# Kernel optimization log

Measured on AMD Instinct MI355X. Metric: run time of the kernel, lower is better.

Reference implementation:

```python
import jax, jax.numpy as jnp
import numpy as np

S, B, D, H, DH = 2048, 2, 512, 8, 64
SCALE = 1.0 / DH ** 0.5
EPS = 1e-5
LN_EPS = 1e-5


def setup_inputs() -> dict:
    key = jax.random.key(0)
    k1, k2, k3, k4 = jax.random.split(key, 4)
    h = jax.random.normal(k1, (S, B, D), dtype=jnp.float32)
    # causal mask, True = masked out, shape [qlen, klen, 1] (dim==3 branch)
    attn_mask = jnp.triu(jnp.ones((S, S), dtype=bool), k=1)[:, :, None]
    Wq = jax.random.normal(k2, (D, H * DH), dtype=jnp.float32) * 0.02
    Wkv = jax.random.normal(k3, (D, 2 * H * DH), dtype=jnp.float32) * 0.02
    Wo = jax.random.normal(k4, (H * DH, D), dtype=jnp.float32) * 0.02
    gamma = jnp.ones((D,), dtype=jnp.float32)
    beta = jnp.zeros((D,), dtype=jnp.float32)
    return {"h": h, "Wq": Wq, "Wkv": Wkv, "Wo": Wo,
            "gamma": gamma, "beta": beta, "attn_mask": attn_mask}


def _layer_norm(x, gamma, beta):
    mu = jnp.mean(x, axis=-1, keepdims=True)
    var = jnp.mean(jnp.square(x - mu), axis=-1, keepdims=True)
    return (x - mu) * jax.lax.rsqrt(var + LN_EPS) * gamma + beta


def reference(h, Wq, Wkv, Wo, gamma, beta, attn_mask):
    # mems=None, pre_lnorm=False, dropout=dropatt=0 (eval)
    c = h
    head_q = (h @ Wq).reshape(S, B, H, DH)
    kv = (c @ Wkv)
    head_k, head_v = jnp.split(kv, 2, axis=-1)
    head_k = head_k.reshape(S, B, H, DH)
    head_v = head_v.reshape(S, B, H, DH)
    # elu(x) + 1 feature map
    head_q = jax.nn.elu(head_q) + 1.0
    head_k = jax.nn.elu(head_k) + 1.0
    # quadratic score matrix [i, j, b, n]
    attn_score = jnp.einsum('ibnd,jbnd->ijbn', head_q, head_k) * SCALE
    # dim==3 mask: [qlen, klen, 1] -> [qlen, klen, 1, 1], fill with 0
    attn_score = jnp.where(attn_mask[:, :, :, None], 0.0, attn_score)
    # sum-normalize over key axis (dim 1 = j)
    denominator = jnp.sum(attn_score, axis=1, keepdims=True) + EPS
    attn_prob = attn_score / denominator
    attn_vec = jnp.einsum('ijbn,jbnd->ibnd', attn_prob, head_v)
    attn_vec = attn_vec.reshape(S, B, H * DH)
    attn_out = attn_vec @ Wo
    # post-lnorm residual
    return _layer_norm(h + attn_out, gamma, beta)
```

## Files before the change

kernel.cpp:

```cpp
#include <hip/hip_runtime.h>
#include <hip/hip_bf16.h>
#include <math.h>

#define SCALE 0.125f
#define EPS 1e-5f
#define LN_EPS 1e-5f

typedef short short8 __attribute__((ext_vector_type(8)));
typedef float floatx4 __attribute__((ext_vector_type(4)));
typedef unsigned short us;

__device__ __forceinline__ float elu1(float x) { return x > 0.f ? x + 1.f : __expf(x); }
__device__ __forceinline__ us f2bf(float f) {
    __hip_bfloat16 b = __float2bfloat16(f);
    return __builtin_bit_cast(us, b);
}
__device__ __forceinline__ void gload_lds16(const void* g, void* lds) {
    __builtin_amdgcn_global_load_lds(
        (const __attribute__((address_space(1))) unsigned int*)g,
        (__attribute__((address_space(3))) unsigned int*)lds, 16, 0, 0);
}
__device__ __forceinline__ floatx4 mfma_bf16(short8 a, short8 b, floatx4 c) {
    return __builtin_amdgcn_mfma_f32_16x16x32_bf16(a, b, c, 0, 0, 0);
}

__global__ __launch_bounds__(256)
void pack_kernel(const float* __restrict__ h, const float* __restrict__ Wq,
                 const float* __restrict__ Wkv, const float* __restrict__ Wo,
                 us* __restrict__ hB, us* __restrict__ WqkvT, us* __restrict__ WoT,
                 us* __restrict__ VTg) {
    const int idx = (blockIdx.x * 256 + threadIdx.x) * 4;
    if (idx < 2097152) {
        float4 v = *(const float4*)(h + idx);
        ushort4 o;
        o.x = f2bf(v.x); o.y = f2bf(v.y); o.z = f2bf(v.z); o.w = f2bf(v.w);
        *(ushort4*)(hB + idx) = o;
    } else if (idx < 2883584) {
        int e = idx - 2097152;
        int n = e >> 9, k = e & 511;
        const float* src; int ld, col;
        if (n < 512) { src = Wq; ld = 512; col = n; }
        else         { src = Wkv; ld = 1024; col = n - 512; }
        ushort4 o;
        o.x = f2bf(src[(size_t)(k + 0) * ld + col]);
        o.y = f2bf(src[(size_t)(k + 1) * ld + col]);
        o.z = f2bf(src[(size_t)(k + 2) * ld + col]);
        o.w = f2bf(src[(size_t)(k + 3) * ld + col]);
        *(ushort4*)(WqkvT + e) = o;
    } else if (idx < 3145728) {
        int e = idx - 2883584;
        int n = e >> 9, k = e & 511;
        ushort4 o;
        o.x = f2bf(Wo[(size_t)(k + 0) * 512 + n]);
        o.y = f2bf(Wo[(size_t)(k + 1) * 512 + n]);
        o.z = f2bf(Wo[(size_t)(k + 2) * 512 + n]);
        o.w = f2bf(Wo[(size_t)(k + 3) * 512 + n]);
        *(ushort4*)(WoT + e) = o;
    } else if (idx < 3178496) {
        int e = idx - 3145728;
        int chain = e >> 11, s = e & 2047;
        ushort4 o; o.x = 0x3f80; o.y = 0x3f80; o.z = 0x3f80; o.w = 0x3f80;
        *(ushort4*)(VTg + ((size_t)(chain * 80 + 64)) * 2048 + s) = o;
    }
}

__global__ __launch_bounds__(256)
void qkv_gemm(const us* __restrict__ A, const us* __restrict__ BT,
              us* __restrict__ Qg, us* __restrict__ Kg, us* __restrict__ Vg) {
    __shared__ __align__(16) us As[128 * 32];
    __shared__ __align__(16) us Bs[128 * 32];
    const int tid = threadIdx.x;
    const int w = tid >> 6, l = tid & 63;
    const int m0 = blockIdx.y * 128, n0 = blockIdx.x * 128;
    const int wm = (w >> 1) * 64, wn = (w & 1) * 64;
    floatx4 acc[4][4];
#pragma unroll
    for (int i = 0; i < 4; ++i)
#pragma unroll
        for (int j = 0; j < 4; ++j)
#pragma unroll
            for (int e = 0; e < 4; ++e) acc[i][j][e] = 0.f;

    for (int kt = 0; kt < 512; kt += 32) {
        __syncthreads();
#pragma unroll
        for (int r = 0; r < 2; ++r) {
            int slot = (r * 4 + w) * 64 + l;
            int row = slot >> 2, part = slot & 3;
            int g = part ^ (row & 3);
            gload_lds16(A + (size_t)(m0 + row) * 512 + kt + g * 8, As + (r * 4 + w) * 512);
            gload_lds16(BT + (size_t)(n0 + row) * 512 + kt + g * 8, Bs + (r * 4 + w) * 512);
        }
        __syncthreads();
        short8 a[4], b[4];
#pragma unroll
        for (int mi = 0; mi < 4; ++mi) {
            int row = wm + mi * 16 + (l & 15);
            int p = (l >> 4) ^ (row & 3);
            a[mi] = *(const short8*)(As + row * 32 + p * 8);
        }
#pragma unroll
        for (int ni = 0; ni < 4; ++ni) {
            int row = wn + ni * 16 + (l & 15);
            int p = (l >> 4) ^ (row & 3);
            b[ni] = *(const short8*)(Bs + row * 32 + p * 8);
        }
#pragma unroll
        for (int mi = 0; mi < 4; ++mi)
#pragma unroll
            for (int ni = 0; ni < 4; ++ni)
                acc[mi][ni] = mfma_bf16(a[mi], b[ni], acc[mi][ni]);
    }
    const int region = blockIdx.x >> 2;
    us* outp = region == 0 ? Qg : (region == 1 ? Kg : Vg);
    const int cb = n0 - region * 512;
#pragma unroll
    for (int mi = 0; mi < 4; ++mi)
#pragma unroll
        for (int ni = 0; ni < 4; ++ni)
#pragma unroll
            for (int r = 0; r < 4; ++r) {
                int row = m0 + wm + mi * 16 + (l >> 4) * 4 + r;
                int col = cb + wn + ni * 16 + (l & 15);
                float v = acc[mi][ni][r];
                if (region < 2) v = elu1(v);
                outp[(size_t)row * 512 + col] = f2bf(v);
            }
}

__global__ __launch_bounds__(256)
void chunk_kv_kernel(const us* __restrict__ Kg, const us* __restrict__ Vg,
                     float* __restrict__ KVc, us* __restrict__ VTg) {
    __shared__ __align__(16) us VT_l[80 * 72];
    __shared__ __align__(16) us KT_l[64 * 72];
    const int c = blockIdx.x, chain = blockIdx.y;
    const int b = chain >> 3, hh = chain & 7;
    const int tid = threadIdx.x;
    const int w = tid >> 6, l = tid & 63;
#pragma unroll
    for (int gi = 0; gi < 2; ++gi) {
        int g = w + gi * 4;
        __align__(16) us vv[8];
        __align__(16) us kk[8];
#pragma unroll
        for (int e = 0; e < 8; ++e) {
            size_t off = (size_t)((c * 64 + g * 8 + e) * 2 + b) * 512 + hh * 64 + l;
            vv[e] = Vg[off];
            kk[e] = Kg[off];
        }
        *(uint4*)(VT_l + l * 72 + g * 8) = *(uint4*)vv;
        *(uint4*)(KT_l + l * 72 + g * 8) = *(uint4*)kk;
        *(uint4*)(VTg + ((size_t)(chain * 80 + l)) * 2048 + c * 64 + g * 8) = *(uint4*)vv;
    }
    if (tid < 8) {
        ushort4 o; o.x = 0x3f80; o.y = 0x3f80; o.z = 0x3f80; o.w = 0x3f80;
        *(ushort4*)(VT_l + 64 * 72 + tid * 8) = o;
        *(ushort4*)(VT_l + 64 * 72 + tid * 8 + 4) = o;
    }
    __syncthreads();
    const int l15 = l & 15, l4 = l >> 4;
    short8 af[5][2], bfr[2];
#pragma unroll
    for (int mi = 0; mi < 5; ++mi) {
        int row = mi * 16 + l15;
        af[mi][0] = *(const short8*)(VT_l + row * 72 + l4 * 8);
        af[mi][1] = *(const short8*)(VT_l + row * 72 + 32 + l4 * 8);
    }
    {
        int row = w * 16 + l15;
        bfr[0] = *(const short8*)(KT_l + row * 72 + l4 * 8);
        bfr[1] = *(const short8*)(KT_l + row * 72 + 32 + l4 * 8);
    }
    float* out = KVc + (size_t)(chain * 32 + c) * 4608;
#pragma unroll
    for (int mi = 0; mi < 5; ++mi) {
        floatx4 a = {0.f, 0.f, 0.f, 0.f};
        a = mfma_bf16(af[mi][0], bfr[0], a);
        a = mfma_bf16(af[mi][1], bfr[1], a);
#pragma unroll
        for (int r = 0; r < 4; ++r) {
            int row = mi * 16 + l4 * 4 + r;
            if (row < 65) out[row * 64 + w * 16 + l15] = a[r];
        }
    }
}

__global__ __launch_bounds__(256)
void cumsum_kernel(const float* __restrict__ KVc, us* __restrict__ MTg) {
    const int chain = blockIdx.x, rg = blockIdx.y;
    const int row = rg * 4 + (threadIdx.x >> 6), col = threadIdx.x & 63;
    const float* in = KVc + (size_t)chain * 32 * 4608 + row * 64 + col;
    us* out = MTg + ((size_t)chain * 32 * 80 + row) * 64 + col;
    float acc = 0.f;
#pragma unroll 4
    for (int cc = 0; cc < 32; ++cc) {
        out[(size_t)cc * 5120] = f2bf(acc);
        acc += in[(size_t)cc * 4608];
    }
}

__global__ __launch_bounds__(256)
void attn_kernel(const us* __restrict__ Qg, const us* __restrict__ Kg,
                 const us* __restrict__ VTg, const us* __restrict__ MTg,
                 us* __restrict__ ATT) {
    __shared__ __align__(16) us Sl[64 * 64];
    const int c = blockIdx.x, chain = blockIdx.y;
    const int b = chain >> 3, hh = chain & 7;
    const int tid = threadIdx.x;
    const int w = tid >> 6, l = tid & 63;
    const int l15 = l & 15, l4 = l >> 4;

    short8 qf[2];
    {
        const us* qb = Qg + ((size_t)((c * 64 + w * 16 + l15) * 2 + b)) * 512 + hh * 64 + l4 * 8;
        qf[0] = *(const short8*)(qb);
        qf[1] = *(const short8*)(qb + 32);
    }
    short8 kf[4][2];
#pragma unroll
    for (int ni = 0; ni < 4; ++ni) {
        const us* kb = Kg + ((size_t)((c * 64 + ni * 16 + l15) * 2 + b)) * 512 + hh * 64 + l4 * 8;
        kf[ni][0] = *(const short8*)(kb);
        kf[ni][1] = *(const short8*)(kb + 32);
    }
    short8 vf[5][2];
#pragma unroll
    for (int ni = 0; ni < 5; ++ni) {
        const us* vb = VTg + ((size_t)(chain * 80 + ni * 16 + l15)) * 2048 + c * 64 + l4 * 8;
        vf[ni][0] = *(const short8*)(vb);
        vf[ni][1] = *(const short8*)(vb + 32);
    }
    short8 mf[5][2];
#pragma unroll
    for (int ni = 0; ni < 5; ++ni) {
        const us* mb = MTg + ((size_t)((chain * 32 + c) * 80 + ni * 16 + l15)) * 64 + l4 * 8;
        mf[ni][0] = *(const short8*)(mb);
        mf[ni][1] = *(const short8*)(mb + 32);
    }

    const int ibase = w * 16 + l4 * 4;
#pragma unroll
    for (int ni = 0; ni < 4; ++ni) {
        floatx4 s = {0.f, 0.f, 0.f, 0.f};
        s = mfma_bf16(qf[0], kf[ni][0], s);
        s = mfma_bf16(qf[1], kf[ni][1], s);
        int col = ni * 16 + l15;
#pragma unroll
        for (int r = 0; r < 4; ++r) {
            int i = ibase + r;
            float v = (col <= i) ? s[r] : 0.f;
            Sl[i * 64 + (((col >> 3) ^ (i & 7)) * 8) + (col & 7)] = f2bf(v);
        }
    }
    __syncthreads();

    short8 sf[2];
    {
        int ir = w * 16 + l15;
        sf[0] = *(const short8*)(Sl + ir * 64 + ((l4 ^ (ir & 7)) * 8));
        sf[1] = *(const short8*)(Sl + ir * 64 + (((4 + l4) ^ (ir & 7)) * 8));
    }

    floatx4 acc[5];
#pragma unroll
    for (int ni = 0; ni < 5; ++ni) {
        floatx4 a = {0.f, 0.f, 0.f, 0.f};
        a = mfma_bf16(sf[0], vf[ni][0], a);
        a = mfma_bf16(sf[1], vf[ni][1], a);
        a = mfma_bf16(qf[0], mf[ni][0], a);
        a = mfma_bf16(qf[1], mf[ni][1], a);
        acc[ni] = a;
    }

    float fac[4];
#pragma unroll
    for (int r = 0; r < 4; ++r) {
        float den = __shfl(acc[4][r], l & 48, 64);
        fac[r] = SCALE / (SCALE * den + EPS);
    }
#pragma unroll
    for (int ni = 0; ni < 4; ++ni)
#pragma unroll
        for (int r = 0; r < 4; ++r) {
            int i = ibase + r;
            ATT[((size_t)((c * 64 + i) * 2 + b)) * 512 + hh * 64 + ni * 16 + l15] =
                f2bf(acc[ni][r] * fac[r]);
        }
}

template <typename OUTT, int ELU_LIM>
__global__ __launch_bounds__(256)
void gemm_mfma(const us* __restrict__ A, const us* __restrict__ BT,
               OUTT* __restrict__ C, int M, int N, int K) {
    __shared__ __align__(16) us As[128 * 32];
    __shared__ __align__(16) us Bs[128 * 32];
    const int tid = threadIdx.x;
    const int w = tid >> 6, l = tid & 63;
    const int m0 = blockIdx.y * 128, n0 = blockIdx.x * 128;
    const int wm = (w >> 1) * 64, wn = (w & 1) * 64;
    floatx4 acc[4][4];
#pragma unroll
    for (int i = 0; i < 4; ++i)
#pragma unroll
        for (int j = 0; j < 4; ++j)
#pragma unroll
            for (int e = 0; e < 4; ++e) acc[i][j][e] = 0.f;
    for (int kt = 0; kt < K; kt += 32) {
        __syncthreads();
#pragma unroll
        for (int r = 0; r < 2; ++r) {
            int slot = (r * 4 + w) * 64 + l;
            int row = slot >> 2, part = slot & 3;
            int g = part ^ (row & 3);
            gload_lds16(A + (size_t)(m0 + row) * K + kt + g * 8, As + (r * 4 + w) * 512);
            gload_lds16(BT + (size_t)(n0 + row) * K + kt + g * 8, Bs + (r * 4 + w) * 512);
        }
        __syncthreads();
        short8 a[4], b[4];
#pragma unroll
        for (int mi = 0; mi < 4; ++mi) {
            int row = wm + mi * 16 + (l & 15);
            int p = (l >> 4) ^ (row & 3);
            a[mi] = *(const short8*)(As + row * 32 + p * 8);
        }
#pragma unroll
        for (int ni = 0; ni < 4; ++ni) {
            int row = wn + ni * 16 + (l & 15);
            int p = (l >> 4) ^ (row & 3);
            b[ni] = *(const short8*)(Bs + row * 32 + p * 8);
        }
#pragma unroll
        for (int mi = 0; mi < 4; ++mi)
#pragma unroll
            for (int ni = 0; ni < 4; ++ni)
                acc[mi][ni] = mfma_bf16(a[mi], b[ni], acc[mi][ni]);
    }
#pragma unroll
    for (int mi = 0; mi < 4; ++mi)
#pragma unroll
        for (int ni = 0; ni < 4; ++ni)
#pragma unroll
            for (int r = 0; r < 4; ++r) {
                int row = m0 + wm + mi * 16 + (l >> 4) * 4 + r;
                int col = n0 + wn + ni * 16 + (l & 15);
                float v = acc[mi][ni][r];
                if (col < ELU_LIM) v = elu1(v);
                if constexpr (sizeof(OUTT) == 2)
                    C[(size_t)row * N + col] = (OUTT)f2bf(v);
                else
                    C[(size_t)row * N + col] = (OUTT)v;
            }
}

__global__ __launch_bounds__(256)
void ln_kernel(const float* __restrict__ h, const float* __restrict__ AO,
               const float* __restrict__ gamma, const float* __restrict__ beta,
               float* __restrict__ out) {
    const int tid = threadIdx.x;
    const int lane = tid & 63, wave = tid >> 6;
    const int row = blockIdx.x * 4 + wave;
    float v[8];
    float sum = 0.f;
#pragma unroll
    for (int i = 0; i < 8; ++i) {
        int col = lane + i * 64;
        float x = h[(size_t)row * 512 + col] + AO[(size_t)row * 512 + col];
        v[i] = x;
        sum += x;
    }
#pragma unroll
    for (int off = 32; off >= 1; off >>= 1) sum += __shfl_xor(sum, off, 64);
    float mean = sum * (1.f / 512);
    float var = 0.f;
#pragma unroll
    for (int i = 0; i < 8; ++i) {
        float d = v[i] - mean;
        var = fmaf(d, d, var);
    }
#pragma unroll
    for (int off = 32; off >= 1; off >>= 1) var += __shfl_xor(var, off, 64);
    float rstd = rsqrtf(var * (1.f / 512) + LN_EPS);
#pragma unroll
    for (int i = 0; i < 8; ++i) {
        int col = lane + i * 64;
        out[(size_t)row * 512 + col] = (v[i] - mean) * rstd * gamma[col] + beta[col];
    }
}

extern "C" void kernel_launch(void* const* d_in, const int* in_sizes, int n_in,
                              void* d_out, int out_size, void* d_ws, size_t ws_size,
                              hipStream_t stream) {
    const float* h = (const float*)d_in[0];
    const float* Wq = (const float*)d_in[1];
    const float* Wkv = (const float*)d_in[2];
    const float* Wo = (const float*)d_in[3];
    const float* gamma = (const float*)d_in[4];
    const float* beta = (const float*)d_in[5];

    char* ws = (char*)d_ws;
    us* Qg      = (us*)(ws + 0);
    us* Kg      = (us*)(ws + 4194304);
    us* Vg      = (us*)(ws + 8388608);
    us* VTg     = (us*)(ws + 12582912);
    us* ATT     = (us*)(ws + 17825792);
    us* WoT     = (us*)(ws + 22020096);
    us* MTg     = (us*)(ws + 22544384);
    us* hB      = (us*)(ws + 27787264);
    us* WqkvT   = (us*)(ws + 31981568);
    float* KVc  = (float*)(ws + 27787264);
    float* AO   = (float*)(ws + 0);

    dim3 blk(256);
    pack_kernel<<<3104, blk, 0, stream>>>(h, Wq, Wkv, Wo, hB, WqkvT, WoT, VTg);
    qkv_gemm<<<dim3(12, 32), blk, 0, stream>>>(hB, WqkvT, Qg, Kg, Vg);
    chunk_kv_kernel<<<dim3(32, 16), blk, 0, stream>>>(Kg, Vg, KVc, VTg);
    cumsum_kernel<<<dim3(16, 17), blk, 0, stream>>>(KVc, MTg);
    attn_kernel<<<dim3(32, 16), blk, 0, stream>>>(Qg, Kg, VTg, MTg, ATT);
    gemm_mfma<float, 0><<<dim3(4, 32), blk, 0, stream>>>(ATT, WoT, AO, 4096, 512, 512);
    ln_kernel<<<1024, blk, 0, stream>>>(h, AO, gamma, beta, (float*)d_out);
}
```

Baseline: 147.1 us.

## Fuse Wo GEMM with LayerNorm, tile weight transpose, stage attention operands in LDS

```diff
diff --git a/kernel.cpp b/kernel.cpp
--- a/kernel.cpp
+++ b/kernel.cpp
@@ -29,35 +29,57 @@
                  const float* __restrict__ Wkv, const float* __restrict__ Wo,
                  us* __restrict__ hB, us* __restrict__ WqkvT, us* __restrict__ WoT,
                  us* __restrict__ VTg) {
-    const int idx = (blockIdx.x * 256 + threadIdx.x) * 4;
-    if (idx < 2097152) {
+    const int bid = blockIdx.x, tid = threadIdx.x;
+    if (bid < 2048) {
+        int idx = bid * 1024 + tid * 4;
         float4 v = *(const float4*)(h + idx);
         ushort4 o;
         o.x = f2bf(v.x); o.y = f2bf(v.y); o.z = f2bf(v.z); o.w = f2bf(v.w);
         *(ushort4*)(hB + idx) = o;
-    } else if (idx < 2883584) {
-        int e = idx - 2097152;
-        int n = e >> 9, k = e & 511;
-        const float* src; int ld, col;
-        if (n < 512) { src = Wq; ld = 512; col = n; }
-        else         { src = Wkv; ld = 1024; col = n - 512; }
-        ushort4 o;
-        o.x = f2bf(src[(size_t)(k + 0) * ld + col]);
-        o.y = f2bf(src[(size_t)(k + 1) * ld + col]);
-        o.z = f2bf(src[(size_t)(k + 2) * ld + col]);
-        o.w = f2bf(src[(size_t)(k + 3) * ld + col]);
-        *(ushort4*)(WqkvT + e) = o;
-    } else if (idx < 3145728) {
-        int e = idx - 2883584;
-        int n = e >> 9, k = e & 511;
-        ushort4 o;
-        o.x = f2bf(Wo[(size_t)(k + 0) * 512 + n]);
-        o.y = f2bf(Wo[(size_t)(k + 1) * 512 + n]);
-        o.z = f2bf(Wo[(size_t)(k + 2) * 512 + n]);
-        o.w = f2bf(Wo[(size_t)(k + 3) * 512 + n]);
-        *(ushort4*)(WoT + e) = o;
-    } else if (idx < 3178496) {
-        int e = idx - 3145728;
+        return;
+    }
+    if (bid < 2304) {
+        __shared__ us T[64][72];
+        const float* src; int ld, n0s, k0; us* dst;
+        if (bid < 2240) {
+            int t2 = bid - 2048;
+            int nt = t2 % 24, kt = t2 / 24;
+            int n0 = nt * 64; k0 = kt * 64;
+            if (n0 < 512) { src = Wq; ld = 512; n0s = n0; }
+            else          { src = Wkv; ld = 1024; n0s = n0 - 512; }
+            dst = WqkvT + (size_t)n0 * 512;
+        } else {
+            int t2 = bid - 2240;
+            int nt = t2 & 7, kt = t2 >> 3;
+            src = Wo; ld = 512; n0s = nt * 64; k0 = kt * 64;
+            dst = WoT + (size_t)(nt * 64) * 512;
+        }
+        {
+            int k = tid >> 2, cs = (tid & 3) * 16;
+            const float* p = src + (size_t)(k0 + k) * ld + n0s + cs;
+#pragma unroll
+            for (int q = 0; q < 4; ++q) {
+                float4 v = *(const float4*)(p + q * 4);
+                T[k][cs + q * 4 + 0] = f2bf(v.x);
+                T[k][cs + q * 4 + 1] = f2bf(v.y);
+                T[k][cs + q * 4 + 2] = f2bf(v.z);
+                T[k][cs + q * 4 + 3] = f2bf(v.w);
+            }
+        }
+        __syncthreads();
+        {
+            int n = tid >> 2, ks = (tid & 3) * 16;
+            __align__(16) us tmp[16];
+#pragma unroll
+            for (int j = 0; j < 16; ++j) tmp[j] = T[ks + j][n];
+            us* po = dst + (size_t)n * 512 + k0 + ks;
+            *(uint4*)(po) = *(uint4*)(tmp);
+            *(uint4*)(po + 8) = *(uint4*)(tmp + 8);
+        }
+        return;
+    }
+    {
+        int e = (bid - 2304) * 1024 + tid * 4;
         int chain = e >> 11, s = e & 2047;
         ushort4 o; o.x = 0x3f80; o.y = 0x3f80; o.z = 0x3f80; o.w = 0x3f80;
         *(ushort4*)(VTg + ((size_t)(chain * 80 + 64)) * 2048 + s) = o;
@@ -203,39 +225,62 @@
 void attn_kernel(const us* __restrict__ Qg, const us* __restrict__ Kg,
                  const us* __restrict__ VTg, const us* __restrict__ MTg,
                  us* __restrict__ ATT) {
+    __shared__ __align__(16) us Qs[64 * 64];
+    __shared__ __align__(16) us Ks[64 * 64];
+    __shared__ __align__(16) us Vs[80 * 64];
+    __shared__ __align__(16) us Ms[80 * 64];
     __shared__ __align__(16) us Sl[64 * 64];
     const int c = blockIdx.x, chain = blockIdx.y;
     const int b = chain >> 3, hh = chain & 7;
     const int tid = threadIdx.x;
     const int w = tid >> 6, l = tid & 63;
     const int l15 = l & 15, l4 = l >> 4;
+    const int lrow = l >> 3, lg = l & 7;
+
+#pragma unroll
+    for (int r = 0; r < 2; ++r) {
+        int slot = r * 4 + w;
+        int row = slot * 8 + lrow;
+        int g = lg ^ (row & 7);
+        size_t grow = (size_t)((c * 64 + row) * 2 + b) * 512 + hh * 64 + g * 8;
+        gload_lds16(Qg + grow, Qs + slot * 512);
+        gload_lds16(Kg + grow, Ks + slot * 512);
+    }
+#pragma unroll
+    for (int r = 0; r < 3; ++r) {
+        int slot = r * 4 + w;
+        if (slot < 10) {
+            int row = slot * 8 + lrow;
+            int g = lg ^ (row & 7);
+            gload_lds16(VTg + (size_t)(chain * 80 + row) * 2048 + c * 64 + g * 8,
+                        Vs + slot * 512);
+            gload_lds16(MTg + ((size_t)(chain * 32 + c) * 80 + row) * 64 + g * 8,
+                        Ms + slot * 512);
+        }
+    }
+    __syncthreads();
 
     short8 qf[2];
     {
-        const us* qb = Qg + ((size_t)((c * 64 + w * 16 + l15) * 2 + b)) * 512 + hh * 64 + l4 * 8;
-        qf[0] = *(const short8*)(qb);
-        qf[1] = *(const short8*)(qb + 32);
+        int row = w * 16 + l15, p = l4 ^ (row & 7);
+        qf[0] = *(const short8*)(Qs + row * 64 + p * 8);
+        qf[1] = *(const short8*)(Qs + row * 64 + (p ^ 4) * 8);
     }
     short8 kf[4][2];
 #pragma unroll
     for (int ni = 0; ni < 4; ++ni) {
-        const us* kb = Kg + ((size_t)((c * 64 + ni * 16 + l15) * 2 + b)) * 512 + hh * 64 + l4 * 8;
-        kf[ni][0] = *(const short8*)(kb);
-        kf[ni][1] = *(const short8*)(kb + 32);
-    }
-    short8 vf[5][2];
+        int row = ni * 16 + l15, p = l4 ^ (row & 7);
+        kf[ni][0] = *(const short8*)(Ks + row * 64 + p * 8);
+        kf[ni][1] = *(const short8*)(Ks + row * 64 + (p ^ 4) * 8);
+    }
+    short8 vf[5][2], mf[5][2];
 #pragma unroll
     for (int ni = 0; ni < 5; ++ni) {
-        const us* vb = VTg + ((size_t)(chain * 80 + ni * 16 + l15)) * 2048 + c * 64 + l4 * 8;
-        vf[ni][0] = *(const short8*)(vb);
-        vf[ni][1] = *(const short8*)(vb + 32);
-    }
-    short8 mf[5][2];
-#pragma unroll
-    for (int ni = 0; ni < 5; ++ni) {
-        const us* mb = MTg + ((size_t)((chain * 32 + c) * 80 + ni * 16 + l15)) * 64 + l4 * 8;
-        mf[ni][0] = *(const short8*)(mb);
-        mf[ni][1] = *(const short8*)(mb + 32);
+        int row = ni * 16 + l15, p = l4 ^ (row & 7);
+        vf[ni][0] = *(const short8*)(Vs + row * 64 + p * 8);
+        vf[ni][1] = *(const short8*)(Vs + row * 64 + (p ^ 4) * 8);
+        mf[ni][0] = *(const short8*)(Ms + row * 64 + p * 8);
+        mf[ni][1] = *(const short8*)(Ms + row * 64 + (p ^ 4) * 8);
     }
 
     const int ibase = w * 16 + l4 * 4;
@@ -288,103 +333,104 @@
         }
 }
 
-template <typename OUTT, int ELU_LIM>
-__global__ __launch_bounds__(256)
-void gemm_mfma(const us* __restrict__ A, const us* __restrict__ BT,
-               OUTT* __restrict__ C, int M, int N, int K) {
-    __shared__ __align__(16) us As[128 * 32];
-    __shared__ __align__(16) us Bs[128 * 32];
+__global__ __launch_bounds__(256)
+void wo_ln_kernel(const us* __restrict__ ATT, const us* __restrict__ WoT,
+                  const float* __restrict__ h, const float* __restrict__ gamma,
+                  const float* __restrict__ beta, float* __restrict__ out) {
+    __shared__ __align__(16) us As[32 * 32];
+    __shared__ __align__(16) us Bs[512 * 32];
+    __shared__ float redS[4][32];
+    __shared__ float redQ[4][32];
+    __shared__ float mml[32], rsl[32];
     const int tid = threadIdx.x;
     const int w = tid >> 6, l = tid & 63;
-    const int m0 = blockIdx.y * 128, n0 = blockIdx.x * 128;
-    const int wm = (w >> 1) * 64, wn = (w & 1) * 64;
-    floatx4 acc[4][4];
-#pragma unroll
-    for (int i = 0; i < 4; ++i)
-#pragma unroll
-        for (int j = 0; j < 4; ++j)
+    const int l15 = l & 15, l4 = l >> 4;
+    const int m0 = blockIdx.x * 32, wn = w * 128;
+    floatx4 acc[2][8];
+#pragma unroll
+    for (int i = 0; i < 2; ++i)
+#pragma unroll
+        for (int j = 0; j < 8; ++j)
 #pragma unroll
             for (int e = 0; e < 4; ++e) acc[i][j][e] = 0.f;
-    for (int kt = 0; kt < K; kt += 32) {
+
+    for (int kt = 0; kt < 512; kt += 32) {
         __syncthreads();
 #pragma unroll
-        for (int r = 0; r < 2; ++r) {
-            int slot = (r * 4 + w) * 64 + l;
-            int row = slot >> 2, part = slot & 3;
-            int g = part ^ (row & 3);
-            gload_lds16(A + (size_t)(m0 + row) * K + kt + g * 8, As + (r * 4 + w) * 512);
-            gload_lds16(BT + (size_t)(n0 + row) * K + kt + g * 8, Bs + (r * 4 + w) * 512);
+        for (int r = 0; r < 8; ++r) {
+            int slot = r * 4 + w;
+            int row = slot * 16 + (l >> 2);
+            int g = (l & 3) ^ (row & 3);
+            gload_lds16(WoT + (size_t)row * 512 + kt + g * 8, Bs + slot * 512);
+        }
+        if (w < 2) {
+            int row = w * 16 + (l >> 2);
+            int g = (l & 3) ^ (row & 3);
+            gload_lds16(ATT + (size_t)(m0 + row) * 512 + kt + g * 8, As + w * 512);
         }
         __syncthreads();
-        short8 a[4], b[4];
-#pragma unroll
-        for (int mi = 0; mi < 4; ++mi) {
-            int row = wm + mi * 16 + (l & 15);
-            int p = (l >> 4) ^ (row & 3);
-            a[mi] = *(const short8*)(As + row * 32 + p * 8);
-        }
-#pragma unroll
-        for (int ni = 0; ni < 4; ++ni) {
-            int row = wn + ni * 16 + (l & 15);
-            int p = (l >> 4) ^ (row & 3);
-            b[ni] = *(const short8*)(Bs + row * 32 + p * 8);
-        }
-#pragma unroll
-        for (int mi = 0; mi < 4; ++mi)
-#pragma unroll
-            for (int ni = 0; ni < 4; ++ni)
-                acc[mi][ni] = mfma_bf16(a[mi], b[ni], acc[mi][ni]);
-    }
-#pragma unroll
-    for (int mi = 0; mi < 4; ++mi)
-#pragma unroll
-        for (int ni = 0; ni < 4; ++ni)
-#pragma unroll
-            for (int r = 0; r < 4; ++r) {
-                int row = m0 + wm + mi * 16 + (l >> 4) * 4 + r;
-                int col = n0 + wn + ni * 16 + (l & 15);
-                float v = acc[mi][ni][r];
-                if (col < ELU_LIM) v = elu1(v);
-                if constexpr (sizeof(OUTT) == 2)
-                    C[(size_t)row * N + col] = (OUTT)f2bf(v);
-                else
-                    C[(size_t)row * N + col] = (OUTT)v;
+        short8 af[2], bf[8];
+#pragma unroll
+        for (int mi = 0; mi < 2; ++mi) {
+            int row = mi * 16 + l15, p = l4 ^ (row & 3);
+            af[mi] = *(const short8*)(As + row * 32 + p * 8);
+        }
+#pragma unroll
+        for (int ni = 0; ni < 8; ++ni) {
+            int row = wn + ni * 16 + l15, p = l4 ^ (row & 3);
+            bf[ni] = *(const short8*)(Bs + row * 32 + p * 8);
+        }
+#pragma unroll
+        for (int mi = 0; mi < 2; ++mi)
+#pragma unroll
+            for (int ni = 0; ni < 8; ++ni)
+                acc[mi][ni] = mfma_bf16(af[mi], bf[ni], acc[mi][ni]);
+    }
+
+#pragma unroll
+    for (int mi = 0; mi < 2; ++mi)
+#pragma unroll
+        for (int r = 0; r < 4; ++r) {
+            int row = mi * 16 + l4 * 4 + r;
+            const float* hrow = h + (size_t)(m0 + row) * 512 + wn + l15;
+            float s = 0.f, q = 0.f;
+#pragma unroll
+            for (int ni = 0; ni < 8; ++ni) {
+                float x = acc[mi][ni][r] + hrow[ni * 16];
+                acc[mi][ni][r] = x;
+                s += x;
+                q = fmaf(x, x, q);
             }
-}
-
-__global__ __launch_bounds__(256)
-void ln_kernel(const float* __restrict__ h, const float* __restrict__ AO,
-               const float* __restrict__ gamma, const float* __restrict__ beta,
-               float* __restrict__ out) {
-    const int tid = threadIdx.x;
-    const int lane = tid & 63, wave = tid >> 6;
-    const int row = blockIdx.x * 4 + wave;
-    float v[8];
-    float sum = 0.f;
-#pragma unroll
-    for (int i = 0; i < 8; ++i) {
-        int col = lane + i * 64;
-        float x = h[(size_t)row * 512 + col] + AO[(size_t)row * 512 + col];
-        v[i] = x;
-        sum += x;
-    }
-#pragma unroll
-    for (int off = 32; off >= 1; off >>= 1) sum += __shfl_xor(sum, off, 64);
-    float mean = sum * (1.f / 512);
-    float var = 0.f;
-#pragma unroll
-    for (int i = 0; i < 8; ++i) {
-        float d = v[i] - mean;
-        var = fmaf(d, d, var);
-    }
-#pragma unroll
-    for (int off = 32; off >= 1; off >>= 1) var += __shfl_xor(var, off, 64);
-    float rstd = rsqrtf(var * (1.f / 512) + LN_EPS);
-#pragma unroll
-    for (int i = 0; i < 8; ++i) {
-        int col = lane + i * 64;
-        out[(size_t)row * 512 + col] = (v[i] - mean) * rstd * gamma[col] + beta[col];
-    }
+#pragma unroll
+            for (int off = 1; off <= 8; off <<= 1) {
+                s += __shfl_xor(s, off, 64);
+                q += __shfl_xor(q, off, 64);
+            }
+            if (l15 == 0) { redS[w][row] = s; redQ[w][row] = q; }
+        }
+    __syncthreads();
+    if (tid < 32) {
+        float s = redS[0][tid] + redS[1][tid] + redS[2][tid] + redS[3][tid];
+        float q = redQ[0][tid] + redQ[1][tid] + redQ[2][tid] + redQ[3][tid];
+        float mean = s * (1.f / 512);
+        float var = q * (1.f / 512) - mean * mean;
+        mml[tid] = mean;
+        rsl[tid] = rsqrtf(var + LN_EPS);
+    }
+    __syncthreads();
+#pragma unroll
+    for (int mi = 0; mi < 2; ++mi)
+#pragma unroll
+        for (int r = 0; r < 4; ++r) {
+            int row = mi * 16 + l4 * 4 + r;
+            float mean = mml[row], rstd = rsl[row];
+#pragma unroll
+            for (int ni = 0; ni < 8; ++ni) {
+                int col = wn + ni * 16 + l15;
+                out[(size_t)(m0 + row) * 512 + col] =
+                    (acc[mi][ni][r] - mean) * rstd * gamma[col] + beta[col];
+            }
+        }
 }
 
 extern "C" void kernel_launch(void* const* d_in, const int* in_sizes, int n_in,
@@ -407,15 +453,13 @@
     us* MTg     = (us*)(ws + 22544384);
     us* hB      = (us*)(ws + 27787264);
     us* WqkvT   = (us*)(ws + 31981568);
-    float* KVc  = (float*)(ws + 27787264);
-    float* AO   = (float*)(ws + 0);
+    float* KVc  = (float*)(ws + 33554432);
 
     dim3 blk(256);
-    pack_kernel<<<3104, blk, 0, stream>>>(h, Wq, Wkv, Wo, hB, WqkvT, WoT, VTg);
+    pack_kernel<<<2336, blk, 0, stream>>>(h, Wq, Wkv, Wo, hB, WqkvT, WoT, VTg);
     qkv_gemm<<<dim3(12, 32), blk, 0, stream>>>(hB, WqkvT, Qg, Kg, Vg);
     chunk_kv_kernel<<<dim3(32, 16), blk, 0, stream>>>(Kg, Vg, KVc, VTg);
     cumsum_kernel<<<dim3(16, 17), blk, 0, stream>>>(KVc, MTg);
     attn_kernel<<<dim3(32, 16), blk, 0, stream>>>(Qg, Kg, VTg, MTg, ATT);
-    gemm_mfma<float, 0><<<dim3(4, 32), blk, 0, stream>>>(ATT, WoT, AO, 4096, 512, 512);
-    ln_kernel<<<1024, blk, 0, stream>>>(h, AO, gamma, beta, (float*)d_out);
-}
+    wo_ln_kernel<<<128, blk, 0, stream>>>(ATT, WoT, h, gamma, beta, (float*)d_out);
+}
```

After: 139.1 us. -5.5%, faster.
